# Optimization experiments

Measured on AMD Instinct MI355X. Metric: run time of the kernel, lower is better.

The kernel has to match this reference:

```python
import jax, jax.numpy as jnp
import numpy as np

K = 3        # kernel size
STRIDE = 1
PAD = 1
DIL = 1


def setup_inputs() -> dict:
    key = jax.random.key(0)
    k1, k2, k3 = jax.random.split(key, 3)
    B, C, H, W, O = 4, 256, 64, 64, 256
    x = jax.random.normal(k1, (B, C, H, W), jnp.float32)
    # offset/mask predictor conv (kaiming-ish small init, zero bias per module init)
    w_off = jax.random.normal(k2, (3 * K * K, C, K, K), jnp.float32) * 0.01
    b_off = jnp.zeros((3 * K * K,), jnp.float32)
    # modulated deformable conv weight (bias=False)
    w_conv = jax.random.normal(k3, (O, C, K, K), jnp.float32) * 0.05
    return {"x": x, "w_off": w_off, "b_off": b_off, "w_conv": w_conv}


def _dfconv(x, w_off, b_off, w_conv):
    B, C, H, W = x.shape
    KK = K * K
    # 1) standard conv predicting offsets+mask: [B, 3*K*K, Ho, Wo]
    om = jax.lax.conv_general_dilated(
        x, w_off, (STRIDE, STRIDE), [(PAD, PAD), (PAD, PAD)],
        rhs_dilation=(DIL, DIL), dimension_numbers=("NCHW", "OIHW", "NCHW"))
    om = om + b_off[None, :, None, None]
    offset = om[:, : 2 * KK]                      # (dy,dx) interleaved per tap
    mask = jax.nn.sigmoid(om[:, 2 * KK:])         # [B, KK, Ho, Wo]
    Ho, Wo = offset.shape[-2:]
    off = offset.reshape(B, KK, 2, Ho, Wo)
    dy, dx = off[:, :, 0], off[:, :, 1]           # [B, KK, Ho, Wo]

    # 2) per-tap sampling coordinates in input space
    ky = jnp.repeat(jnp.arange(K), K).astype(x.dtype)   # tap row index [KK]
    kx = jnp.tile(jnp.arange(K), K).astype(x.dtype)     # tap col index [KK]
    base_y = (jnp.arange(Ho) * STRIDE - PAD).astype(x.dtype)
    base_x = (jnp.arange(Wo) * STRIDE - PAD).astype(x.dtype)
    py = dy + base_y[None, None, :, None] + (ky * DIL)[None, :, None, None]
    px = dx + base_x[None, None, None, :] + (kx * DIL)[None, :, None, None]

    # 3) bilinear sample with zero padding outside the image
    y0f = jnp.floor(py)
    x0f = jnp.floor(px)
    wy = py - y0f
    wx = px - x0f
    y0 = y0f.astype(jnp.int32)
    x0 = x0f.astype(jnp.int32)
    img = x.reshape(B, C, H * W)

    def gather(yi, xi):
        valid = ((yi >= 0) & (yi < H) & (xi >= 0) & (xi < W)).astype(x.dtype)
        idx = jnp.clip(yi, 0, H - 1) * W + jnp.clip(xi, 0, W - 1)
        g = jnp.take_along_axis(img, idx.reshape(B, 1, -1), axis=2)
        return g.reshape(B, C, KK, Ho, Wo) * valid[:, None]

    wy_ = wy[:, None]  # [B,1,KK,Ho,Wo]
    wx_ = wx[:, None]
    val = (gather(y0, x0) * (1 - wy_) * (1 - wx_)
           + gather(y0, x0 + 1) * (1 - wy_) * wx_
           + gather(y0 + 1, x0) * wy_ * (1 - wx_)
           + gather(y0 + 1, x0 + 1) * wy_ * wx_)

    # 4) modulation + weighted accumulation over taps and channels
    val = val * mask[:, None]                      # [B,C,KK,Ho,Wo]
    out = jnp.einsum("bckhw,ock->bohw", val, w_conv.reshape(w_conv.shape[0], C, KK))
    return out


def reference(x, w_off, b_off, w_conv):
    return _dfconv(x, w_off, b_off, w_conv)
```

## Files before the change

### kernel.cpp

```cpp
#include <hip/hip_runtime.h>
#include <hip/hip_bf16.h>

#define XH   64
#define XW   64
#define CIN  256
#define COUT 256
#define BATCH 4
#define KK9  9
#define M_TOT 16384
#define K_TOT 2304
#define NKSTEP 36

typedef __attribute__((ext_vector_type(8))) short short8;
typedef __attribute__((ext_vector_type(4))) short short4v;
typedef __attribute__((ext_vector_type(4))) float f32x4;

#define OM_OFF   0
#define OM_BYTES (BATCH*27*4096*4)
#define XT_OFF   (OM_OFF + OM_BYTES)
#define XT_BYTES (BATCH*4096*CIN*2)
#define WT_OFF   (XT_OFF + XT_BYTES)
#define WT_BYTES (COUT*K_TOT*2)
#define WOT_OFF  (WT_OFF + WT_BYTES)
#define WOT_BYTES (36*32*64*2)

__device__ __forceinline__ void async16(const void* g, void* l) {
  __builtin_amdgcn_global_load_lds((const __attribute__((address_space(1))) void*)g,
                                   (__attribute__((address_space(3))) void*)l,
                                   16, 0, 0);
}

__device__ __forceinline__ float b2f(short s) {
  union { float f; unsigned u; } x;
  x.u = ((unsigned)(unsigned short)s) << 16;
  return x.f;
}

struct Taps { short8 t00, t01, t10, t11; };

__global__ __launch_bounds__(256) void k0_wt(const float* __restrict__ wconv,
                                             __hip_bfloat16* __restrict__ Wt3) {
  int e = blockIdx.x * 256 + threadIdx.x;
  int j3   = e & 7;
  int lane = (e >> 3) & 63;
  int kc   = (e >> 9) & 1;
  int og   = (e >> 10) & 15;
  int tk   = e >> 14;
  int o = og * 16 + (lane & 15);
  int k = tk * 64 + kc * 32 + ((lane >> 4) << 3) + j3;
  int kk = k >> 8, c = k & 255;
  float v = wconv[(o * CIN + c) * KK9 + kk];
  Wt3[e] = __float2bfloat16(v);
}

__global__ __launch_bounds__(256) void k0b_wot(const float* __restrict__ woff,
                                               __hip_bfloat16* __restrict__ Wot) {
  int e = blockIdx.x * 256 + threadIdx.x;
  int tk = e >> 11;
  int r  = e & 2047;
  int ocl = r >> 6, j = r & 63;
  int kl = j ^ ((ocl & 7) << 3);
  int k = tk * 64 + kl;
  int kk = k >> 8, c = k & 255;
  float v = (ocl < 27) ? woff[((size_t)(ocl * 256 + c)) * 9 + kk] : 0.f;
  Wot[e] = __float2bfloat16(v);
}

__global__ __launch_bounds__(256) void kt_xt(const float* __restrict__ x,
                                             __hip_bfloat16* __restrict__ xTh) {
  __shared__ float t[64][65];
  int blk = blockIdx.x;
  int hwg = blk & 63;
  int cg  = (blk >> 6) & 3;
  int b   = blk >> 8;
  int hw0 = hwg * 64, c0 = cg * 64;
  int l = threadIdx.x & 63, q = threadIdx.x >> 6;
  const float* xb = x + ((size_t)(b * 256 + c0) << 12) + hw0;
#pragma unroll
  for (int i = 0; i < 16; ++i) {
    int cl = q * 16 + i;
    t[cl][l] = xb[((size_t)cl << 12) + l];
  }
  __syncthreads();
  __hip_bfloat16* xTb = xTh + (((size_t)b << 12) + hw0) * 256 + c0;
#pragma unroll
  for (int i = 0; i < 16; ++i) {
    int hwl = q * 16 + i;
    xTb[(size_t)hwl * 256 + l] = __float2bfloat16(t[l][hwl]);
  }
}

__global__ __launch_bounds__(256) void k1_omgemm(const __hip_bfloat16* __restrict__ xTh,
                                                 const __hip_bfloat16* __restrict__ Wot,
                                                 const float* __restrict__ boff,
                                                 float* __restrict__ om) {
  __shared__ __align__(16) __hip_bfloat16 sP[32 * 64];
  __shared__ __align__(16) __hip_bfloat16 sWo[32 * 64];
  int bid = blockIdx.x;
  int tm = ((bid & 7) << 6) | (bid >> 3);
  int tid = threadIdx.x;
  int wv = tid >> 6, lane = tid & 63;
  int lo = lane & 15, hi = lane >> 4;
  int wr = wv >> 1, wc = wv & 1;

  int row = tid >> 3;
  int kb  = (tid & 7) * 8;
  int colz = kb ^ ((row & 7) << 3);

  int m_s = tm * 32 + row;
  int b_s = m_s >> 12, hw_s = m_s & 4095, h_s = hw_s >> 6, w_s = hw_s & 63;

  f32x4 acc = {0.f, 0.f, 0.f, 0.f};

  for (int tk = 0; tk < NKSTEP; ++tk) {
    async16((const char*)Wot + (size_t)tk * 4096 + tid * 16, (char*)sWo + tid * 16);

    int kk = tk >> 2, cc = tk & 3;
    int ky = kk / 3, kx = kk - ky * 3;
    int yy = h_s + ky - 1, xx = w_s + kx - 1;
    bool valid = ((unsigned)yy < 64u) && ((unsigned)xx < 64u);
    short8 h8 = {0, 0, 0, 0, 0, 0, 0, 0};
    if (valid)
      h8 = *(const short8*)(xTh + ((((size_t)b_s << 12) + yy * 64 + xx) << 8) + cc * 64 + kb);
    *(short8*)&sP[row * 64 + colz] = h8;
    __syncthreads();

#pragma unroll
    for (int kc = 0; kc < 2; ++kc) {
      int cz = (kc * 32 + hi * 8) ^ ((lo & 7) << 3);
      short8 bfr = *(const short8*)&sP[(wr * 16 + lo) * 64 + cz];
      short8 a   = *(const short8*)&sWo[(wc * 16 + lo) * 64 + cz];
      acc = __builtin_amdgcn_mfma_f32_16x16x32_bf16(a, bfr, acc, 0, 0, 0);
    }
    __syncthreads();
  }

  int m_o = tm * 32 + wr * 16 + lo;
  int b_o = m_o >> 12, hw_o = m_o & 4095;
#pragma unroll
  for (int r = 0; r < 4; ++r) {
    int oc = wc * 16 + hi * 4 + r;
    if (oc < 27)
      om[(((size_t)(b_o * 27 + oc)) << 12) + hw_o] = acc[r] + boff[oc];
  }
}

__global__ __launch_bounds__(256, 2) void k23_fused(const __hip_bfloat16* __restrict__ xTh,
                                                    const float* __restrict__ om,
                                                    const __hip_bfloat16* __restrict__ Wt3,
                                                    float* __restrict__ out) {
  __shared__ __align__(16) __hip_bfloat16 sV[2][32 * 64];
  __shared__ float sw00[288], sw01[288], sw10[288], sw11[288];
  __shared__ int   so00[288], so01[288], so10[288], so11[288];

  int bid = blockIdx.x;
  int tm = ((bid & 7) << 6) | (bid >> 3);
  int tid = threadIdx.x;
  int wv = tid >> 6, lane = tid & 63;
  int lo = lane & 15, hi = lane >> 4;
  int b = tm >> 7;
  int m0 = tm * 32;

  for (int it = tid; it < 288; it += 256) {
    int kk = it >> 5, row = it & 31;
    int m = m0 + row;
    int hw = m & 4095, h = hw >> 6, w = hw & 63;
    const float* omb = om + ((size_t)(b * 27) << 12) + hw;
    float dy = omb[(size_t)(2 * kk) << 12];
    float dx = omb[(size_t)(2 * kk + 1) << 12];
    float mz = omb[(size_t)(18 + kk) << 12];
    int ky = kk / 3, kx = kk - ky * 3;
    float py = dy + (float)(h - 1 + ky);
    float px = dx + (float)(w - 1 + kx);
    float y0f = floorf(py), x0f = floorf(px);
    float wy = py - y0f, wx = px - x0f;
    int y0 = (int)y0f, x0 = (int)x0f;
    bool vy0 = (unsigned)y0 < 64u, vy1 = (unsigned)(y0 + 1) < 64u;
    bool vx0 = (unsigned)x0 < 64u, vx1 = (unsigned)(x0 + 1) < 64u;
    int cy0 = min(max(y0, 0), 63), cy1 = min(max(y0 + 1, 0), 63);
    int cx0 = min(max(x0, 0), 63), cx1 = min(max(x0 + 1, 0), 63);
    float mask = 1.f / (1.f + __expf(-mz));
    sw00[it] = (vy0 && vx0) ? (1.f - wy) * (1.f - wx) * mask : 0.f;
    sw01[it] = (vy0 && vx1) ? (1.f - wy) * wx * mask : 0.f;
    sw10[it] = (vy1 && vx0) ? wy * (1.f - wx) * mask : 0.f;
    sw11[it] = (vy1 && vx1) ? wy * wx * mask : 0.f;
    so00[it] = cy0 * 64 + cx0;
    so01[it] = cy0 * 64 + cx1;
    so10[it] = cy1 * 64 + cx0;
    so11[it] = cy1 * 64 + cx1;
  }
  __syncthreads();

  const __hip_bfloat16* xb = xTh + ((size_t)b << 20);
  int vrow = tid >> 3;
  int chq  = tid & 7;
  int colz = (chq * 8) ^ ((vrow & 7) << 3);

  auto loadTaps = [&](int tkq, Taps& T) {
    int it = (tkq >> 2) * 32 + vrow;
    const __hip_bfloat16* base = xb + (tkq & 3) * 64 + chq * 8;
    T.t00 = *(const short8*)(base + (size_t)so00[it] * 256);
    T.t01 = *(const short8*)(base + (size_t)so01[it] * 256);
    T.t10 = *(const short8*)(base + (size_t)so10[it] * 256);
    T.t11 = *(const short8*)(base + (size_t)so11[it] * 256);
  };
  auto buildV = [&](int tkq, const Taps& T, int buf) {
    int it = (tkq >> 2) * 32 + vrow;
    float a00 = sw00[it], a01 = sw01[it], a10 = sw10[it], a11 = sw11[it];
    __hip_bfloat16 h8[8];
#pragma unroll
    for (int j = 0; j < 8; ++j) {
      float v = a00 * b2f(T.t00[j]) + a01 * b2f(T.t01[j])
              + a10 * b2f(T.t10[j]) + a11 * b2f(T.t11[j]);
      h8[j] = __float2bfloat16(v);
    }
    *(short8*)&sV[buf][vrow * 64 + colz] = *(const short8*)h8;
  };
  auto loadW = [&](int tkq, short8 (&aw)[8]) {
#pragma unroll
    for (int fo = 0; fo < 4; ++fo)
#pragma unroll
      for (int kc = 0; kc < 2; ++kc)
        aw[fo * 2 + kc] = *(const short8*)((const char*)Wt3
                          + ((((size_t)tkq * 16 + (wv * 4 + fo)) * 2 + kc) << 10)
                          + lane * 16);
  };

  f32x4 zero4 = {0.f, 0.f, 0.f, 0.f};
  f32x4 acc[4][2];
#pragma unroll
  for (int fo = 0; fo < 4; ++fo)
#pragma unroll
    for (int fm = 0; fm < 2; ++fm) acc[fo][fm] = zero4;

  Taps TA, TB;
  short8 awA[8], awB[8];
  loadW(0, awA);
  loadTaps(0, TA);
  buildV(0, TA, 0);
  loadTaps(1, TB);
  asm volatile("s_waitcnt lgkmcnt(0)" ::: "memory");
  __builtin_amdgcn_s_barrier();

  auto body = [&](int tk, Taps& Tuse, Taps& Tload,
                  short8 (&awUse)[8], short8 (&awLoad)[8]) {
    int cb = tk & 1, nb = cb ^ 1;
    bool more1 = (tk + 1 < NKSTEP), more2 = (tk + 2 < NKSTEP);
    if (more1) loadW(tk + 1, awLoad);
    if (more2) loadTaps(tk + 2, Tload);
    if (more1) buildV(tk + 1, Tuse, nb);

    __builtin_amdgcn_s_setprio(1);
#pragma unroll
    for (int kc = 0; kc < 2; ++kc) {
      int cz = (kc * 32 + hi * 8) ^ ((lo & 7) << 3);
      short8 bv[2];
#pragma unroll
      for (int fm = 0; fm < 2; ++fm)
        bv[fm] = *(const short8*)&sV[cb][(fm * 16 + lo) * 64 + cz];
#pragma unroll
      for (int fo = 0; fo < 4; ++fo)
#pragma unroll
        for (int fm = 0; fm < 2; ++fm)
          acc[fo][fm] = __builtin_amdgcn_mfma_f32_16x16x32_bf16(awUse[fo * 2 + kc], bv[fm], acc[fo][fm], 0, 0, 0);
    }
    __builtin_amdgcn_s_setprio(0);

    if (more1) {
      asm volatile("s_waitcnt lgkmcnt(0)" ::: "memory");
      __builtin_amdgcn_s_barrier();
    }
  };

  for (int tkp = 0; tkp < NKSTEP; tkp += 2) {
    body(tkp,     TB, TA, awA, awB);
    body(tkp + 1, TA, TB, awB, awA);
  }

  int hwbase = m0 & 4095;
#pragma unroll
  for (int fo = 0; fo < 4; ++fo) {
    int o = wv * 64 + fo * 16 + hi * 4;
#pragma unroll
    for (int fm = 0; fm < 2; ++fm) {
      int mloc = hwbase + fm * 16 + lo;
#pragma unroll
      for (int r = 0; r < 4; ++r)
        out[((size_t)(b * 256 + o + r)) * 4096 + mloc] = acc[fo][fm][r];
    }
  }
}

extern "C" void kernel_launch(void* const* d_in, const int* in_sizes, int n_in,
                              void* d_out, int out_size, void* d_ws, size_t ws_size,
                              hipStream_t stream) {
  (void)in_sizes; (void)n_in; (void)out_size; (void)ws_size;
  const float* x     = (const float*)d_in[0];
  const float* woff  = (const float*)d_in[1];
  const float* boff  = (const float*)d_in[2];
  const float* wconv = (const float*)d_in[3];
  char* ws = (char*)d_ws;
  float* om   = (float*)(ws + OM_OFF);
  __hip_bfloat16* xTh = (__hip_bfloat16*)(ws + XT_OFF);
  __hip_bfloat16* Wt3 = (__hip_bfloat16*)(ws + WT_OFF);
  __hip_bfloat16* Wot = (__hip_bfloat16*)(ws + WOT_OFF);
  float* out = (float*)d_out;

  hipLaunchKernelGGL(k0_wt,     dim3(2304), dim3(256), 0, stream, wconv, Wt3);
  hipLaunchKernelGGL(k0b_wot,   dim3(288),  dim3(256), 0, stream, woff, Wot);
  hipLaunchKernelGGL(kt_xt,     dim3(1024), dim3(256), 0, stream, x, xTh);
  hipLaunchKernelGGL(k1_omgemm, dim3(512),  dim3(256), 0, stream, xTh, Wot, boff, om);
  hipLaunchKernelGGL(k23_fused, dim3(512),  dim3(256), 0, stream, xTh, om, Wt3, out);
}
```

Baseline: 74.94 us.

## Fuse offset/mask conv GEMM into deformable conv kernel via shared memory

Removes the separate offset/mask GEMM kernel and computes the 27-channel offset/mask tile inside the fused deformable conv kernel. Results go to shared memory instead of a global om buffer. The offset weights are re-laid out into MFMA fragment order so they load directly into registers, and patch loads are double-buffered through the shared V buffer. This saves a kernel launch and the global round trip of om. The cost is a longer serial prologue in each block before the main GEMM starts.

```diff
diff --git a/kernel.cpp b/kernel.cpp
--- a/kernel.cpp
+++ b/kernel.cpp
@@ -12,23 +12,14 @@
 #define NKSTEP 36
 
 typedef __attribute__((ext_vector_type(8))) short short8;
-typedef __attribute__((ext_vector_type(4))) short short4v;
 typedef __attribute__((ext_vector_type(4))) float f32x4;
 
-#define OM_OFF   0
-#define OM_BYTES (BATCH*27*4096*4)
-#define XT_OFF   (OM_OFF + OM_BYTES)
+#define XT_OFF   0
 #define XT_BYTES (BATCH*4096*CIN*2)
 #define WT_OFF   (XT_OFF + XT_BYTES)
 #define WT_BYTES (COUT*K_TOT*2)
 #define WOT_OFF  (WT_OFF + WT_BYTES)
-#define WOT_BYTES (36*32*64*2)
-
-__device__ __forceinline__ void async16(const void* g, void* l) {
-  __builtin_amdgcn_global_load_lds((const __attribute__((address_space(1))) void*)g,
-                                   (__attribute__((address_space(3))) void*)l,
-                                   16, 0, 0);
-}
+#define WOT_BYTES (36*2*2*64*8*2)
 
 __device__ __forceinline__ float b2f(short s) {
   union { float f; unsigned u; } x;
@@ -54,16 +45,18 @@
 }
 
 __global__ __launch_bounds__(256) void k0b_wot(const float* __restrict__ woff,
-                                               __hip_bfloat16* __restrict__ Wot) {
+                                               __hip_bfloat16* __restrict__ Wot3) {
   int e = blockIdx.x * 256 + threadIdx.x;
-  int tk = e >> 11;
-  int r  = e & 2047;
-  int ocl = r >> 6, j = r & 63;
-  int kl = j ^ ((ocl & 7) << 3);
-  int k = tk * 64 + kl;
+  int j3   = e & 7;
+  int lane = (e >> 3) & 63;
+  int kc   = (e >> 9) & 1;
+  int wc   = (e >> 10) & 1;
+  int tk   = e >> 11;
+  int oc = wc * 16 + (lane & 15);
+  int k = tk * 64 + kc * 32 + ((lane >> 4) << 3) + j3;
   int kk = k >> 8, c = k & 255;
-  float v = (ocl < 27) ? woff[((size_t)(ocl * 256 + c)) * 9 + kk] : 0.f;
-  Wot[e] = __float2bfloat16(v);
+  float v = (oc < 27) ? woff[((size_t)(oc * 256 + c)) * 9 + kk] : 0.f;
+  Wot3[e] = __float2bfloat16(v);
 }
 
 __global__ __launch_bounds__(256) void kt_xt(const float* __restrict__ x,
@@ -90,66 +83,13 @@
   }
 }
 
-__global__ __launch_bounds__(256) void k1_omgemm(const __hip_bfloat16* __restrict__ xTh,
-                                                 const __hip_bfloat16* __restrict__ Wot,
-                                                 const float* __restrict__ boff,
-                                                 float* __restrict__ om) {
-  __shared__ __align__(16) __hip_bfloat16 sP[32 * 64];
-  __shared__ __align__(16) __hip_bfloat16 sWo[32 * 64];
-  int bid = blockIdx.x;
-  int tm = ((bid & 7) << 6) | (bid >> 3);
-  int tid = threadIdx.x;
-  int wv = tid >> 6, lane = tid & 63;
-  int lo = lane & 15, hi = lane >> 4;
-  int wr = wv >> 1, wc = wv & 1;
-
-  int row = tid >> 3;
-  int kb  = (tid & 7) * 8;
-  int colz = kb ^ ((row & 7) << 3);
-
-  int m_s = tm * 32 + row;
-  int b_s = m_s >> 12, hw_s = m_s & 4095, h_s = hw_s >> 6, w_s = hw_s & 63;
-
-  f32x4 acc = {0.f, 0.f, 0.f, 0.f};
-
-  for (int tk = 0; tk < NKSTEP; ++tk) {
-    async16((const char*)Wot + (size_t)tk * 4096 + tid * 16, (char*)sWo + tid * 16);
-
-    int kk = tk >> 2, cc = tk & 3;
-    int ky = kk / 3, kx = kk - ky * 3;
-    int yy = h_s + ky - 1, xx = w_s + kx - 1;
-    bool valid = ((unsigned)yy < 64u) && ((unsigned)xx < 64u);
-    short8 h8 = {0, 0, 0, 0, 0, 0, 0, 0};
-    if (valid)
-      h8 = *(const short8*)(xTh + ((((size_t)b_s << 12) + yy * 64 + xx) << 8) + cc * 64 + kb);
-    *(short8*)&sP[row * 64 + colz] = h8;
-    __syncthreads();
-
-#pragma unroll
-    for (int kc = 0; kc < 2; ++kc) {
-      int cz = (kc * 32 + hi * 8) ^ ((lo & 7) << 3);
-      short8 bfr = *(const short8*)&sP[(wr * 16 + lo) * 64 + cz];
-      short8 a   = *(const short8*)&sWo[(wc * 16 + lo) * 64 + cz];
-      acc = __builtin_amdgcn_mfma_f32_16x16x32_bf16(a, bfr, acc, 0, 0, 0);
-    }
-    __syncthreads();
-  }
-
-  int m_o = tm * 32 + wr * 16 + lo;
-  int b_o = m_o >> 12, hw_o = m_o & 4095;
-#pragma unroll
-  for (int r = 0; r < 4; ++r) {
-    int oc = wc * 16 + hi * 4 + r;
-    if (oc < 27)
-      om[(((size_t)(b_o * 27 + oc)) << 12) + hw_o] = acc[r] + boff[oc];
-  }
-}
-
 __global__ __launch_bounds__(256, 2) void k23_fused(const __hip_bfloat16* __restrict__ xTh,
-                                                    const float* __restrict__ om,
                                                     const __hip_bfloat16* __restrict__ Wt3,
+                                                    const __hip_bfloat16* __restrict__ Wot3,
+                                                    const float* __restrict__ boff,
                                                     float* __restrict__ out) {
-  __shared__ __align__(16) __hip_bfloat16 sV[2][32 * 64];
+  __shared__ __align__(16) __hip_bfloat16 sPV[2][32 * 64];
+  __shared__ float sOM[32][32];
   __shared__ float sw00[288], sw01[288], sw10[288], sw11[288];
   __shared__ int   so00[288], so01[288], so10[288], so11[288];
 
@@ -161,14 +101,80 @@
   int b = tm >> 7;
   int m0 = tm * 32;
 
+  {
+    int wr = wv >> 1, wc = wv & 1;
+    int prow = tid >> 3;
+    int pkb  = (tid & 7) * 8;
+    int pcolz = pkb ^ ((prow & 7) << 3);
+    int m_s = m0 + prow;
+    int hw_s = m_s & 4095, h_s = hw_s >> 6, w_s = hw_s & 63;
+
+    auto loadPatch = [&](int tkq) -> short8 {
+      int kk = tkq >> 2, cc = tkq & 3;
+      int ky = kk / 3, kx = kk - ky * 3;
+      int yy = h_s + ky - 1, xx = w_s + kx - 1;
+      short8 h8 = {0, 0, 0, 0, 0, 0, 0, 0};
+      if (((unsigned)yy < 64u) && ((unsigned)xx < 64u))
+        h8 = *(const short8*)(xTh + ((((size_t)b << 12) + yy * 64 + xx) << 8) + cc * 64 + pkb);
+      return h8;
+    };
+    auto loadWot = [&](int tkq, short8 (&w2)[2]) {
+#pragma unroll
+      for (int kc = 0; kc < 2; ++kc)
+        w2[kc] = *(const short8*)((const char*)Wot3
+                  + ((((size_t)tkq * 2 + wc) * 2 + kc) << 10) + lane * 16);
+    };
+
+    f32x4 acc1 = {0.f, 0.f, 0.f, 0.f};
+    short8 PA, PB, wUA[2], wUB[2];
+    PA = loadPatch(0);
+    loadWot(0, wUA);
+    *(short8*)&sPV[0][prow * 64 + pcolz] = PA;
+    PB = loadPatch(1);
+    asm volatile("s_waitcnt lgkmcnt(0)" ::: "memory");
+    __builtin_amdgcn_s_barrier();
+
+    auto p1body = [&](int tk, short8& Puse, short8& Pload,
+                      short8 (&wU)[2], short8 (&wL)[2]) {
+      int cb = tk & 1, nb = cb ^ 1;
+      bool more1 = (tk + 1 < NKSTEP), more2 = (tk + 2 < NKSTEP);
+      if (more1) {
+        loadWot(tk + 1, wL);
+        *(short8*)&sPV[nb][prow * 64 + pcolz] = Puse;
+      }
+      if (more2) Pload = loadPatch(tk + 2);
+#pragma unroll
+      for (int kc = 0; kc < 2; ++kc) {
+        int cz = (kc * 32 + hi * 8) ^ ((lo & 7) << 3);
+        short8 bfr = *(const short8*)&sPV[cb][(wr * 16 + lo) * 64 + cz];
+        acc1 = __builtin_amdgcn_mfma_f32_16x16x32_bf16(wU[kc], bfr, acc1, 0, 0, 0);
+      }
+      if (more1) {
+        asm volatile("s_waitcnt lgkmcnt(0)" ::: "memory");
+        __builtin_amdgcn_s_barrier();
+      }
+    };
+    for (int tkp = 0; tkp < NKSTEP; tkp += 2) {
+      p1body(tkp,     PB, PA, wUA, wUB);
+      p1body(tkp + 1, PA, PB, wUB, wUA);
+    }
+
+    int oc0 = wc * 16 + hi * 4;
+#pragma unroll
+    for (int r = 0; r < 4; ++r) {
+      float bias = (oc0 + r < 27) ? boff[oc0 + r] : 0.f;
+      sOM[wr * 16 + lo][oc0 + r] = acc1[r] + bias;
+    }
+  }
+  __syncthreads();
+
   for (int it = tid; it < 288; it += 256) {
     int kk = it >> 5, row = it & 31;
     int m = m0 + row;
     int hw = m & 4095, h = hw >> 6, w = hw & 63;
-    const float* omb = om + ((size_t)(b * 27) << 12) + hw;
-    float dy = omb[(size_t)(2 * kk) << 12];
-    float dx = omb[(size_t)(2 * kk + 1) << 12];
-    float mz = omb[(size_t)(18 + kk) << 12];
+    float dy = sOM[row][2 * kk];
+    float dx = sOM[row][2 * kk + 1];
+    float mz = sOM[row][18 + kk];
     int ky = kk / 3, kx = kk - ky * 3;
     float py = dy + (float)(h - 1 + ky);
     float px = dx + (float)(w - 1 + kx);
@@ -214,7 +220,7 @@
               + a10 * b2f(T.t10[j]) + a11 * b2f(T.t11[j]);
       h8[j] = __float2bfloat16(v);
     }
-    *(short8*)&sV[buf][vrow * 64 + colz] = *(const short8*)h8;
+    *(short8*)&sPV[buf][vrow * 64 + colz] = *(const short8*)h8;
   };
   auto loadW = [&](int tkq, short8 (&aw)[8]) {
 #pragma unroll
@@ -257,7 +263,7 @@
       short8 bv[2];
 #pragma unroll
       for (int fm = 0; fm < 2; ++fm)
-        bv[fm] = *(const short8*)&sV[cb][(fm * 16 + lo) * 64 + cz];
+        bv[fm] = *(const short8*)&sPV[cb][(fm * 16 + lo) * 64 + cz];
 #pragma unroll
       for (int fo = 0; fo < 4; ++fo)
 #pragma unroll
@@ -300,15 +306,13 @@
   const float* boff  = (const float*)d_in[2];
   const float* wconv = (const float*)d_in[3];
   char* ws = (char*)d_ws;
-  float* om   = (float*)(ws + OM_OFF);
-  __hip_bfloat16* xTh = (__hip_bfloat16*)(ws + XT_OFF);
-  __hip_bfloat16* Wt3 = (__hip_bfloat16*)(ws + WT_OFF);
-  __hip_bfloat16* Wot = (__hip_bfloat16*)(ws + WOT_OFF);
+  __hip_bfloat16* xTh  = (__hip_bfloat16*)(ws + XT_OFF);
+  __hip_bfloat16* Wt3  = (__hip_bfloat16*)(ws + WT_OFF);
+  __hip_bfloat16* Wot3 = (__hip_bfloat16*)(ws + WOT_OFF);
   float* out = (float*)d_out;
 
   hipLaunchKernelGGL(k0_wt,     dim3(2304), dim3(256), 0, stream, wconv, Wt3);
-  hipLaunchKernelGGL(k0b_wot,   dim3(288),  dim3(256), 0, stream, woff, Wot);
+  hipLaunchKernelGGL(k0b_wot,   dim3(288),  dim3(256), 0, stream, woff, Wot3);
   hipLaunchKernelGGL(kt_xt,     dim3(1024), dim3(256), 0, stream, x, xTh);
-  hipLaunchKernelGGL(k1_omgemm, dim3(512),  dim3(256), 0, stream, xTh, Wot, boff, om);
-  hipLaunchKernelGGL(k23_fused, dim3(512),  dim3(256), 0, stream, xTh, om, Wt3, out);
-}
+  hipLaunchKernelGGL(k23_fused, dim3(512),  dim3(256), 0, stream, xTh, Wt3, Wot3, boff, out);
+}
```

Measured after the change: 69.20 us. 7.7% less time.
